# Performance work log

Measured on AMD Instinct MI355X. Metric: run time of the kernel, lower is better.

Reference implementation:

```python
import jax, jax.numpy as jnp
import numpy as np

EPS = 1e-8


def setup_inputs() -> dict:
    key = jax.random.key(0)
    k1, k2, k3 = jax.random.split(key, 3)
    n_nodes, n_pos, d, n_seg = 50000, 2048, 128, 32
    pred = jax.random.normal(k1, (n_nodes, d), dtype=jnp.float32)
    target = jax.random.normal(k2, (n_pos, d), dtype=jnp.float32)
    target_identifiers = jax.random.randint(k3, (n_pos,), 0, n_seg, dtype=jnp.int64)
    return {
        "pred": pred,
        "target": target,
        "target_identifiers": target_identifiers,
        "num_segments": n_seg,
    }


def reference(pred, target, target_identifiers, num_segments):
    # Pairwise L2 distance: sqrt(||t||^2 - 2 t.p + ||p||^2 + eps)
    # avoids materializing the [n_pos, n_nodes, d] broadcast tensor.
    t2 = jnp.sum(target * target, axis=-1, keepdims=True)          # [n_pos, 1]
    p2 = jnp.sum(pred * pred, axis=-1)                             # [n_nodes]
    cross = jnp.einsum('pd,nd->pn', target, pred)                  # [n_pos, n_nodes]
    sq = jnp.maximum(t2 - 2.0 * cross + p2[None, :], 0.0)
    dist_mat = jnp.sqrt(sq + EPS)                                  # [n_pos, n_nodes]

    # stage1: scatter_mean over target_identifiers (dim=0)
    seg_sum = jax.ops.segment_sum(dist_mat, target_identifiers,
                                  num_segments=num_segments)       # [n_seg, n_nodes]
    counts = jax.ops.segment_sum(jnp.ones((dist_mat.shape[0],), dist_mat.dtype),
                                 target_identifiers, num_segments=num_segments)
    seg_mean = seg_sum / jnp.maximum(counts, 1.0)[:, None]

    # stage2: mean over segments
    return seg_mean.mean(axis=0)                                   # [n_nodes]
```

## Files before the change

### kernel.cpp

```cpp
#include <hip/hip_runtime.h>

#define DIMK 128

typedef __bf16 bf16x8 __attribute__((ext_vector_type(8)));
typedef float  f32x4  __attribute__((ext_vector_type(4)));

__device__ inline unsigned short f32_to_bf16_rne(float f) {
    unsigned u = __float_as_uint(f);
    u += 0x7FFFu + ((u >> 16) & 1u);
    return (unsigned short)(u >> 16);
}


__global__ void pack_rows(const float* __restrict__ src,
                          unsigned short* __restrict__ dst,
                          float* __restrict__ norm2,
                          int n_valid, int n_rows_pad) {
    int wave = threadIdx.x >> 6, lane = threadIdx.x & 63;
    int row = blockIdx.x * 4 + wave;
    if (row >= n_rows_pad) return;
    int srow = min(row, n_valid - 1);
    int e = lane * 2;
    float2 v = *(const float2*)(src + (size_t)srow * DIMK + e);
    unsigned pk = (unsigned)f32_to_bf16_rne(v.x) |
                  ((unsigned)f32_to_bf16_rne(v.y) << 16);
    int tile = row >> 4, col = row & 15;
    int kk = e >> 5, kb = (e >> 3) & 3, j = e & 7;
    size_t off = (size_t)tile * 2048 + kk * 512 + (kb * 16 + col) * 8 + j;
    *(unsigned*)(dst + off) = pk;
    float s = v.x * v.x + v.y * v.y;
#pragma unroll
    for (int o = 1; o < 64; o <<= 1) s += __shfl_xor(s, o, 64);
    if (lane == 0) norm2[row] = s;
}

__global__ void seg_weights(const int* __restrict__ ids,
                            const int* __restrict__ nseg_p,
                            const float* __restrict__ t2,
                            float2* __restrict__ tw, int n_pos) {
    __shared__ int   cnt[256];
    __shared__ float w[256];
    int nseg = nseg_p[0];
    if (nseg > 256) nseg = 256;
    int t = threadIdx.x;
    if (t < nseg) cnt[t] = 0;
    __syncthreads();
    for (int p = t; p < n_pos; p += blockDim.x) atomicAdd(&cnt[ids[p]], 1);
    __syncthreads();
    if (t < nseg) w[t] = 1.0f / ((float)nseg * (float)max(cnt[t], 1));
    __syncthreads();
    for (int p = t; p < n_pos; p += blockDim.x) {
        float2 e; e.x = t2[p]; e.y = w[ids[p]];
        tw[p] = e;
    }
}

__global__ __launch_bounds__(256)
void l2dist_main(const unsigned short* __restrict__ pb,
                 const float* __restrict__ p2,
                 const unsigned short* __restrict__ tb,
                 const float2* __restrict__ tw,
                 float* __restrict__ out,
                 int n_nodes, int tiles) {
    __shared__ __align__(16) unsigned short lbuf[2][2048];
    const int lane = threadIdx.x & 63;
    const int wave = threadIdx.x >> 6;
    const int col  = lane & 15;
    const int kb   = lane >> 4;
    const int n0   = blockIdx.x * 128 + wave * 32;

    bf16x8 bfrag[2][4];
    float p2g[2];
    const unsigned short* bp = pb + ((size_t)(n0 >> 4)) * 2048 + (size_t)lane * 8;
#pragma unroll
    for (int g = 0; g < 2; ++g) {
#pragma unroll
        for (int kk = 0; kk < 4; ++kk)
            bfrag[g][kk] = *(const bf16x8*)(bp + g * 2048 + kk * 512);
        p2g[g] = p2[n0 + g * 16 + col];
    }

    const int pbase = blockIdx.y * tiles;
    const unsigned short* sp = tb + (size_t)pbase * 2048 + wave * 512 + lane * 8;
    unsigned short* ld0 = &lbuf[0][wave * 512];
    unsigned short* ld1 = &lbuf[1][wave * 512];
    const float2* twp = tw + ((size_t)pbase << 4) + kb * 4;

    __builtin_amdgcn_global_load_lds(
        (const __attribute__((address_space(1))) unsigned int*)(const void*)sp,
        (__attribute__((address_space(3))) unsigned int*)(void*)ld0, 16, 0, 0);
    sp += 2048;
    f32x4 cw0 = *(const f32x4*)(twp);
    f32x4 cw1 = *(const f32x4*)(twp + 2);
    twp += 16;

    float acc0 = 0.f, acc1 = 0.f;

    for (int t = 0; t < tiles; ++t) {
        asm volatile("s_waitcnt vmcnt(0)" ::: "memory");
        __syncthreads();

        if (t + 1 < tiles) {
            __builtin_amdgcn_global_load_lds(
                (const __attribute__((address_space(1))) unsigned int*)(const void*)sp,
                (__attribute__((address_space(3))) unsigned int*)(void*)((t & 1) ? ld0 : ld1),
                16, 0, 0);
            sp += 2048;
        }
        f32x4 nw0 = cw0, nw1 = cw1;
        if (t + 1 < tiles) {
            nw0 = *(const f32x4*)(twp);
            nw1 = *(const f32x4*)(twp + 2);
            twp += 16;
        }

        const unsigned short* rb = &lbuf[t & 1][lane * 8];
        bf16x8 a0 = *(const bf16x8*)(rb);
        bf16x8 a1 = *(const bf16x8*)(rb + 512);
        bf16x8 a2 = *(const bf16x8*)(rb + 1024);
        bf16x8 a3 = *(const bf16x8*)(rb + 1536);

        f32x4 d0 = {0.f, 0.f, 0.f, 0.f};
        f32x4 d1 = {0.f, 0.f, 0.f, 0.f};
        d0 = __builtin_amdgcn_mfma_f32_16x16x32_bf16(a0, bfrag[0][0], d0, 0, 0, 0);
        d1 = __builtin_amdgcn_mfma_f32_16x16x32_bf16(a0, bfrag[1][0], d1, 0, 0, 0);
        d0 = __builtin_amdgcn_mfma_f32_16x16x32_bf16(a1, bfrag[0][1], d0, 0, 0, 0);
        d1 = __builtin_amdgcn_mfma_f32_16x16x32_bf16(a1, bfrag[1][1], d1, 0, 0, 0);
        d0 = __builtin_amdgcn_mfma_f32_16x16x32_bf16(a2, bfrag[0][2], d0, 0, 0, 0);
        d1 = __builtin_amdgcn_mfma_f32_16x16x32_bf16(a2, bfrag[1][2], d1, 0, 0, 0);
        d0 = __builtin_amdgcn_mfma_f32_16x16x32_bf16(a3, bfrag[0][3], d0, 0, 0, 0);
        d1 = __builtin_amdgcn_mfma_f32_16x16x32_bf16(a3, bfrag[1][3], d1, 0, 0, 0);

        float t2v[4] = {cw0[0], cw0[2], cw1[0], cw1[2]};
        float wv[4]  = {cw0[1], cw0[3], cw1[1], cw1[3]};
#pragma unroll
        for (int j = 0; j < 4; ++j) {
            float s0 = fmaf(-2.f, d0[j], t2v[j] + p2g[0]);
            float s1 = fmaf(-2.f, d1[j], t2v[j] + p2g[1]);
            acc0 = fmaf(wv[j], __builtin_amdgcn_sqrtf(fmaxf(s0, 0.f)), acc0);
            acc1 = fmaf(wv[j], __builtin_amdgcn_sqrtf(fmaxf(s1, 0.f)), acc1);
        }
        cw0 = nw0; cw1 = nw1;
    }

    acc0 += __shfl_xor(acc0, 16, 64);
    acc0 += __shfl_xor(acc0, 32, 64);
    acc1 += __shfl_xor(acc1, 16, 64);
    acc1 += __shfl_xor(acc1, 32, 64);
    if (lane < 16) {
        int na = n0 + col;
        int nb = n0 + 16 + col;
        if (na < n_nodes) atomicAdd(out + na, acc0);
        if (nb < n_nodes) atomicAdd(out + nb, acc1);
    }
}

extern "C" void kernel_launch(void* const* d_in, const int* in_sizes, int n_in,
                              void* d_out, int out_size, void* d_ws, size_t ws_size,
                              hipStream_t stream) {
    const float* pred  = (const float*)d_in[0];
    const float* tgt   = (const float*)d_in[1];
    const int*   ids   = (const int*)d_in[2];
    const int*   nsegp = (const int*)d_in[3];
    float* out = (float*)d_out;

    int n_nodes = in_sizes[0] / DIMK;
    int n_pos   = in_sizes[2];

    int gx = (n_nodes + 127) / 128;
    int n_rows_pad = gx * 128;

    char* ws = (char*)d_ws;
    size_t off_pb = 0;
    size_t off_tb = off_pb + (size_t)n_rows_pad * DIMK * 2;
    size_t off_p2 = off_tb + (size_t)n_pos * DIMK * 2;
    size_t off_t2 = off_p2 + (size_t)n_rows_pad * 4;
    size_t off_tw = off_t2 + (size_t)n_pos * 4;
    unsigned short* pb = (unsigned short*)(ws + off_pb);
    unsigned short* tb = (unsigned short*)(ws + off_tb);
    float*          p2 = (float*)(ws + off_p2);
    float*          t2 = (float*)(ws + off_t2);
    float2*         tw = (float2*)(ws + off_tw);

    pack_rows<<<(n_rows_pad + 3) / 4, 256, 0, stream>>>(pred, pb, p2, n_nodes, n_rows_pad);
    pack_rows<<<(n_pos + 3) / 4, 256, 0, stream>>>(tgt, tb, t2, n_pos, n_pos);
    seg_weights<<<1, 1024, 0, stream>>>(ids, nsegp, t2, tw, n_pos);
    hipMemsetAsync(out, 0, (size_t)out_size * sizeof(float), stream);

    const int YS = 8;
    int tiles = (n_pos >> 4) / YS;
    dim3 grid(gx, YS);
    l2dist_main<<<grid, 256, 0, stream>>>(pb, p2, tb, tw, out, n_nodes, tiles);
}
```

Before: 61.89 us.

## Split target rows into small slices loaded fully into LDS per block

Restructures the main kernel so each block handles a fixed slice of 8 target tiles, all loaded into LDS at once, instead of 16 tiles streamed through a double buffer. The grid's y dimension grows from 8 to n_pos/128 (16 for these inputs), which adds blocks but also re-reads each pred fragment from global memory and doubles the atomic adds per output. It also folds the -2 factor into the bf16 target packing to save a multiply per element. Segment weights are staged in LDS, and launch bounds request higher occupancy.

Measured after the change: 58.94 us. 4.8% less time.

```diff
diff --git a/kernel.cpp b/kernel.cpp
--- a/kernel.cpp
+++ b/kernel.cpp
@@ -15,15 +15,15 @@
 __global__ void pack_rows(const float* __restrict__ src,
                           unsigned short* __restrict__ dst,
                           float* __restrict__ norm2,
-                          int n_valid, int n_rows_pad) {
+                          int n_valid, int n_rows_pad, float scale) {
     int wave = threadIdx.x >> 6, lane = threadIdx.x & 63;
     int row = blockIdx.x * 4 + wave;
     if (row >= n_rows_pad) return;
     int srow = min(row, n_valid - 1);
     int e = lane * 2;
     float2 v = *(const float2*)(src + (size_t)srow * DIMK + e);
-    unsigned pk = (unsigned)f32_to_bf16_rne(v.x) |
-                  ((unsigned)f32_to_bf16_rne(v.y) << 16);
+    unsigned pk = (unsigned)f32_to_bf16_rne(scale * v.x) |
+                  ((unsigned)f32_to_bf16_rne(scale * v.y) << 16);
     int tile = row >> 4, col = row & 15;
     int kk = e >> 5, kb = (e >> 3) & 3, j = e & 7;
     size_t off = (size_t)tile * 2048 + kk * 512 + (kb * 16 + col) * 8 + j;
@@ -55,16 +55,20 @@
     }
 }
 
-__global__ __launch_bounds__(256)
+#define SLICE_TILES 8
+__global__ __launch_bounds__(256, 4)
 void l2dist_main(const unsigned short* __restrict__ pb,
                  const float* __restrict__ p2,
                  const unsigned short* __restrict__ tb,
                  const float2* __restrict__ tw,
                  float* __restrict__ out,
-                 int n_nodes, int tiles) {
-    __shared__ __align__(16) unsigned short lbuf[2][2048];
-    const int lane = threadIdx.x & 63;
-    const int wave = threadIdx.x >> 6;
+                 int n_nodes) {
+    __shared__ __align__(16) unsigned short lbuf[SLICE_TILES][2048];
+    __shared__ __align__(16) float tw_lds[SLICE_TILES * 32];
+
+    const int tid  = threadIdx.x;
+    const int lane = tid & 63;
+    const int wave = tid >> 6;
     const int col  = lane & 15;
     const int kb   = lane >> 4;
     const int n0   = blockIdx.x * 128 + wave * 32;
@@ -80,41 +84,31 @@
         p2g[g] = p2[n0 + g * 16 + col];
     }
 
-    const int pbase = blockIdx.y * tiles;
-    const unsigned short* sp = tb + (size_t)pbase * 2048 + wave * 512 + lane * 8;
-    unsigned short* ld0 = &lbuf[0][wave * 512];
-    unsigned short* ld1 = &lbuf[1][wave * 512];
-    const float2* twp = tw + ((size_t)pbase << 4) + kb * 4;
+    const int pbase = blockIdx.y * SLICE_TILES;
 
-    __builtin_amdgcn_global_load_lds(
-        (const __attribute__((address_space(1))) unsigned int*)(const void*)sp,
-        (__attribute__((address_space(3))) unsigned int*)(void*)ld0, 16, 0, 0);
-    sp += 2048;
-    f32x4 cw0 = *(const f32x4*)(twp);
-    f32x4 cw1 = *(const f32x4*)(twp + 2);
-    twp += 16;
+    if (tid < SLICE_TILES * 16) {
+        float2 e = tw[pbase * 16 + tid];
+        tw_lds[2 * tid]     = e.x;
+        tw_lds[2 * tid + 1] = e.y;
+    }
+
+    const unsigned short* sgp = tb + (size_t)pbase * 2048 + wave * 512 + lane * 8;
+    unsigned short* ldst = &lbuf[0][0] + wave * 512;
+#pragma unroll
+    for (int t = 0; t < SLICE_TILES; ++t) {
+        __builtin_amdgcn_global_load_lds(
+            (const __attribute__((address_space(1))) unsigned int*)(const void*)
+                (sgp + (size_t)t * 2048),
+            (__attribute__((address_space(3))) unsigned int*)(void*)
+                (ldst + t * 2048),
+            16, 0, 0);
+    }
+    __syncthreads();
 
     float acc0 = 0.f, acc1 = 0.f;
-
-    for (int t = 0; t < tiles; ++t) {
-        asm volatile("s_waitcnt vmcnt(0)" ::: "memory");
-        __syncthreads();
-
-        if (t + 1 < tiles) {
-            __builtin_amdgcn_global_load_lds(
-                (const __attribute__((address_space(1))) unsigned int*)(const void*)sp,
-                (__attribute__((address_space(3))) unsigned int*)(void*)((t & 1) ? ld0 : ld1),
-                16, 0, 0);
-            sp += 2048;
-        }
-        f32x4 nw0 = cw0, nw1 = cw1;
-        if (t + 1 < tiles) {
-            nw0 = *(const f32x4*)(twp);
-            nw1 = *(const f32x4*)(twp + 2);
-            twp += 16;
-        }
-
-        const unsigned short* rb = &lbuf[t & 1][lane * 8];
+#pragma unroll
+    for (int t = 0; t < SLICE_TILES; ++t) {
+        const unsigned short* rb = &lbuf[t][lane * 8];
         bf16x8 a0 = *(const bf16x8*)(rb);
         bf16x8 a1 = *(const bf16x8*)(rb + 512);
         bf16x8 a2 = *(const bf16x8*)(rb + 1024);
@@ -131,16 +125,17 @@
         d0 = __builtin_amdgcn_mfma_f32_16x16x32_bf16(a3, bfrag[0][3], d0, 0, 0, 0);
         d1 = __builtin_amdgcn_mfma_f32_16x16x32_bf16(a3, bfrag[1][3], d1, 0, 0, 0);
 
-        float t2v[4] = {cw0[0], cw0[2], cw1[0], cw1[2]};
-        float wv[4]  = {cw0[1], cw0[3], cw1[1], cw1[3]};
+        f32x4 w0 = *(const f32x4*)&tw_lds[(t * 16 + kb * 4) * 2];
+        f32x4 w1 = *(const f32x4*)&tw_lds[(t * 16 + kb * 4) * 2 + 4];
+        float t2v[4] = {w0[0], w0[2], w1[0], w1[2]};
+        float wv[4]  = {w0[1], w0[3], w1[1], w1[3]};
 #pragma unroll
         for (int j = 0; j < 4; ++j) {
-            float s0 = fmaf(-2.f, d0[j], t2v[j] + p2g[0]);
-            float s1 = fmaf(-2.f, d1[j], t2v[j] + p2g[1]);
+            float s0 = d0[j] + (t2v[j] + p2g[0]);
+            float s1 = d1[j] + (t2v[j] + p2g[1]);
             acc0 = fmaf(wv[j], __builtin_amdgcn_sqrtf(fmaxf(s0, 0.f)), acc0);
             acc1 = fmaf(wv[j], __builtin_amdgcn_sqrtf(fmaxf(s1, 0.f)), acc1);
         }
-        cw0 = nw0; cw1 = nw1;
     }
 
     acc0 += __shfl_xor(acc0, 16, 64);
@@ -182,13 +177,12 @@
     float*          t2 = (float*)(ws + off_t2);
     float2*         tw = (float2*)(ws + off_tw);
 
-    pack_rows<<<(n_rows_pad + 3) / 4, 256, 0, stream>>>(pred, pb, p2, n_nodes, n_rows_pad);
-    pack_rows<<<(n_pos + 3) / 4, 256, 0, stream>>>(tgt, tb, t2, n_pos, n_pos);
+    pack_rows<<<(n_rows_pad + 3) / 4, 256, 0, stream>>>(pred, pb, p2, n_nodes, n_rows_pad, 1.0f);
+    pack_rows<<<(n_pos + 3) / 4, 256, 0, stream>>>(tgt, tb, t2, n_pos, n_pos, -2.0f);
     seg_weights<<<1, 1024, 0, stream>>>(ids, nsegp, t2, tw, n_pos);
     hipMemsetAsync(out, 0, (size_t)out_size * sizeof(float), stream);
 
-    const int YS = 8;
-    int tiles = (n_pos >> 4) / YS;
-    dim3 grid(gx, YS);
-    l2dist_main<<<grid, 256, 0, stream>>>(pb, p2, tb, tw, out, n_nodes, tiles);
+    int ys = (n_pos >> 4) / SLICE_TILES;
+    dim3 grid(gx, ys);
+    l2dist_main<<<grid, 256, 0, stream>>>(pb, p2, tb, tw, out, n_nodes);
 }
```
